# Optimization experiments

Hardware: AMD Instinct MI355X
Metric: run time of the kernel (lower is better)

Reference implementation:

```python
import jax, jax.numpy as jnp
import numpy as np

EPS = 1e-5

def _ln(x, w, b):
    m = jnp.mean(x, axis=-1, keepdims=True)
    v = jnp.var(x, axis=-1, keepdims=True)
    return (x - m) * jax.lax.rsqrt(v + EPS) * w + b

def setup_inputs() -> dict:
    key = jax.random.key(0)
    ks = jax.random.split(key, 8)
    B, N, C, H, D, Hid = 8, 1024, 1024, 16, 64, 4096
    s_in = 1.0 / np.sqrt(C)
    s_out = 1.0 / np.sqrt(Hid + C)
    return {
        "x": jax.random.normal(ks[0], (B, N, C), jnp.float32),
        "in_norm_w": jnp.ones((C,), jnp.float32),
        "in_norm_b": jnp.zeros((C,), jnp.float32),
        "in_proj_w": jax.random.normal(ks[1], (Hid + 3 * C, C), jnp.float32) * s_in,
        "mlp_bias": jax.random.normal(ks[2], (Hid,), jnp.float32) * 0.02,
        "q_norm_w": jnp.ones((D,), jnp.float32),
        "q_norm_b": jnp.zeros((D,), jnp.float32),
        "k_norm_w": jnp.ones((D,), jnp.float32),
        "k_norm_b": jnp.zeros((D,), jnp.float32),
        "out_proj_w": jax.random.normal(ks[3], (2 * C, Hid + C), jnp.float32) * s_out,
        "out_proj_b": jax.random.normal(ks[4], (2 * C,), jnp.float32) * 0.02,
        "ls_gamma": jnp.full((C,), 1e-5, jnp.float32),
    }

def reference(x, in_norm_w, in_norm_b, in_proj_w, mlp_bias,
              q_norm_w, q_norm_b, k_norm_w, k_norm_b,
              out_proj_w, out_proj_b, ls_gamma):
    B, N, C = x.shape
    Hid = mlp_bias.shape[0]
    H = 16
    D = C // H
    y = _ln(x, in_norm_w, in_norm_b)
    # faithful to source: bias = cat(qkv_zeros[3C], mlp_bias) despite split order (mlp, q, k, v)
    bias = jnp.concatenate([jnp.zeros((3 * C,), x.dtype), mlp_bias])
    z = jnp.einsum('bnc,oc->bno', y, in_proj_w) + bias
    x_mlp = z[..., :Hid]
    q = z[..., Hid:Hid + C].reshape(B, N, H, D)
    k = z[..., Hid + C:Hid + 2 * C].reshape(B, N, H, D)
    v = z[..., Hid + 2 * C:].reshape(B, N, H, D)
    q = _ln(q, q_norm_w, q_norm_b).transpose(0, 2, 1, 3)  # [B,H,N,D]
    k = _ln(k, k_norm_w, k_norm_b).transpose(0, 2, 1, 3)
    v = v.transpose(0, 2, 1, 3)
    scale = 1.0 / np.sqrt(D)
    scores = jnp.einsum('bhnd,bhmd->bhnm', q, k) * scale
    attn = jax.nn.softmax(scores, axis=-1)
    x_attn = jnp.einsum('bhnm,bhmd->bhnd', attn, v)
    x_attn = x_attn.transpose(0, 2, 1, 3).reshape(B, N, C)
    x_mlp = jax.nn.gelu(x_mlp, approximate=False)
    cat = jnp.concatenate([x_mlp, x_attn], axis=-1)  # [B,N,Hid+C]
    out = jnp.einsum('bnf,of->bno', cat, out_proj_w) + out_proj_b
    x_mlp_out, x_attn_out = out[..., :C], out[..., C:]
    return x + ls_gamma * (x_attn_out + x_mlp_out)
```

## Files before the change

### kernel.cpp

```cpp
#include <hip/hip_runtime.h>
#include <math.h>


typedef __bf16 bf16x8 __attribute__((ext_vector_type(8)));
typedef float f32x4 __attribute__((ext_vector_type(4)));
typedef unsigned short ushort8v __attribute__((ext_vector_type(8)));

#define GLD16(g, l)                                                            \
  __builtin_amdgcn_global_load_lds(                                            \
      (const __attribute__((address_space(1))) void*)(g),                      \
      (__attribute__((address_space(3))) void*)(l), 16, 0, 0)

__device__ __forceinline__ float b2f(unsigned short u) {
  union { unsigned int i; float f; } v;
  v.i = ((unsigned int)u) << 16;
  return v.f;
}
__device__ __forceinline__ unsigned short f2b(float f) {
  unsigned int i = __float_as_uint(f);
  return (unsigned short)((i + 0x7fffu + ((i >> 16) & 1u)) >> 16);
}
__device__ __forceinline__ unsigned short cvt_elem(const void* p, int i, bool f32) {
  return f32 ? f2b(((const float*)p)[i]) : ((const unsigned short*)p)[i];
}

#define P_INW 0
#define P_INB 1024
#define P_MLPB 2048
#define P_QW 6144
#define P_QB 6208
#define P_KW 6272
#define P_KB 6336

__global__ __launch_bounds__(1024) void k_small(
    const void* inw, const void* inb, const void* mlpb, const void* qw,
    const void* qb, const void* kw, const void* kb,
    unsigned short* __restrict__ params) {
  int t = threadIdx.x;
  bool f32 = (((const unsigned short*)inw)[0] == 0);
  params[P_INW + t] = cvt_elem(inw, t, f32);
  params[P_INB + t] = cvt_elem(inb, t, f32);
  for (int i = t; i < 4096; i += 1024) params[P_MLPB + i] = cvt_elem(mlpb, i, f32);
  if (t < 64) {
    params[P_QW + t] = cvt_elem(qw, t, f32);
    params[P_QB + t] = cvt_elem(qb, t, f32);
    params[P_KW + t] = cvt_elem(kw, t, f32);
    params[P_KB + t] = cvt_elem(kb, t, f32);
  }
}

__global__ __launch_bounds__(256) void k_cvt(
    const void* __restrict__ src, unsigned short* __restrict__ dst, int n4,
    const unsigned short* __restrict__ probe) {
  int i = blockIdx.x * 256 + threadIdx.x;
  if (i >= n4) return;
  bool f32 = (probe[0] == 0);
  if (f32) {
    float4 v = ((const float4*)src)[i];
    ushort4 o;
    o.x = f2b(v.x); o.y = f2b(v.y); o.z = f2b(v.z); o.w = f2b(v.w);
    ((ushort4*)dst)[i] = o;
  } else {
    ((ushort4*)dst)[i] = ((const ushort4*)src)[i];
  }
}

__global__ __launch_bounds__(256) void k_wsum(
    const void* __restrict__ W2, const void* __restrict__ ob,
    unsigned short* __restrict__ W2s, float* __restrict__ bsum,
    const unsigned short* __restrict__ probe) {
  int i = blockIdx.x * 256 + threadIdx.x;
  bool f32 = (probe[0] == 0);
  const int half4 = 1310720;
  if (f32) {
    float4 a = ((const float4*)W2)[i];
    float4 b = ((const float4*)W2)[i + half4];
    ushort4 o;
    o.x = f2b(a.x + b.x); o.y = f2b(a.y + b.y);
    o.z = f2b(a.z + b.z); o.w = f2b(a.w + b.w);
    ((ushort4*)W2s)[i] = o;
    if (i < 1024) bsum[i] = ((const float*)ob)[i] + ((const float*)ob)[i + 1024];
  } else {
    ushort4 a = ((const ushort4*)W2)[i];
    ushort4 b = ((const ushort4*)W2)[i + half4];
    ushort4 o;
    o.x = f2b(b2f(a.x) + b2f(b.x)); o.y = f2b(b2f(a.y) + b2f(b.y));
    o.z = f2b(b2f(a.z) + b2f(b.z)); o.w = f2b(b2f(a.w) + b2f(b.w));
    ((ushort4*)W2s)[i] = o;
    if (i < 1024)
      bsum[i] = b2f(((const unsigned short*)ob)[i]) +
                b2f(((const unsigned short*)ob)[i + 1024]);
  }
}

__global__ __launch_bounds__(256) void k_ln_in(
    const void* __restrict__ x, const unsigned short* __restrict__ params,
    unsigned short* __restrict__ y, const unsigned short* __restrict__ probe) {
  int row = blockIdx.x;
  int t = threadIdx.x;
  bool f32 = (probe[0] == 0);
  float v0, v1, v2, v3;
  if (f32) {
    float4 u = *(const float4*)((const float*)x + (size_t)row * 1024u + t * 4);
    v0 = u.x; v1 = u.y; v2 = u.z; v3 = u.w;
  } else {
    ushort4 u = *(const ushort4*)((const unsigned short*)x + (size_t)row * 1024u + t * 4);
    v0 = b2f(u.x); v1 = b2f(u.y); v2 = b2f(u.z); v3 = b2f(u.w);
  }
  float s = v0 + v1 + v2 + v3;
  float s2 = v0 * v0 + v1 * v1 + v2 * v2 + v3 * v3;
  for (int off = 32; off; off >>= 1) {
    s += __shfl_down(s, off);
    s2 += __shfl_down(s2, off);
  }
  __shared__ __align__(16) float red[8];
  int wv = t >> 6, ln = t & 63;
  if (ln == 0) { red[wv] = s; red[4 + wv] = s2; }
  __syncthreads();
  float S = red[0] + red[1] + red[2] + red[3];
  float S2 = red[4] + red[5] + red[6] + red[7];
  float mean = S * (1.0f / 1024.0f);
  float var = S2 * (1.0f / 1024.0f) - mean * mean;
  float rs = rsqrtf(var + 1e-5f);
  ushort4 wv4 = *(const ushort4*)(params + P_INW + t * 4);
  ushort4 bv4 = *(const ushort4*)(params + P_INB + t * 4);
  ushort4 o;
  o.x = f2b((v0 - mean) * rs * b2f(wv4.x) + b2f(bv4.x));
  o.y = f2b((v1 - mean) * rs * b2f(wv4.y) + b2f(bv4.y));
  o.z = f2b((v2 - mean) * rs * b2f(wv4.z) + b2f(bv4.z));
  o.w = f2b((v3 - mean) * rs * b2f(wv4.w) + b2f(bv4.w));
  *(ushort4*)(y + (size_t)row * 1024u + t * 4) = o;
}

__global__ __launch_bounds__(256) void k_gemm1(
    const unsigned short* __restrict__ A, const unsigned short* __restrict__ W,
    const unsigned short* __restrict__ params, unsigned short* __restrict__ Z,
    int ldz, int mode) {
  __shared__ __align__(16) unsigned short As[128 * 32];
  __shared__ __align__(16) unsigned short Bs[128 * 32];
  const int K = 1024;
  int m0 = blockIdx.x * 128, n0 = blockIdx.y * 128;
  int t = threadIdx.x;
  int wv = t >> 6, lane = t & 63, q4 = lane >> 4, l15 = lane & 15;
  int wm = (wv >> 1) * 64, wn = (wv & 1) * 64;
  f32x4 acc[4][4];
  f32x4 z4 = {0.f, 0.f, 0.f, 0.f};
#pragma unroll
  for (int i = 0; i < 4; i++)
#pragma unroll
    for (int j = 0; j < 4; j++) acc[i][j] = z4;

  const unsigned short* a0 = A + (size_t)(m0 + (t >> 2)) * K + (t & 3) * 8;
  const unsigned short* a1 = a0 + (size_t)64 * K;
  const unsigned short* b0 = W + (size_t)(n0 + (t >> 2)) * K + (t & 3) * 8;
  const unsigned short* b1 = b0 + (size_t)64 * K;

  for (int k0 = 0; k0 < K; k0 += 32) {
    GLD16(a0 + k0, As + t * 8);
    GLD16(a1 + k0, As + (t + 256) * 8);
    GLD16(b0 + k0, Bs + t * 8);
    GLD16(b1 + k0, Bs + (t + 256) * 8);
    __syncthreads();
    bf16x8 af[4], bfv[4];
#pragma unroll
    for (int mi = 0; mi < 4; mi++)
      af[mi] = *(const bf16x8*)(As + (wm + mi * 16 + l15) * 32 + q4 * 8);
#pragma unroll
    for (int ni = 0; ni < 4; ni++)
      bfv[ni] = *(const bf16x8*)(Bs + (wn + ni * 16 + l15) * 32 + q4 * 8);
#pragma unroll
    for (int mi = 0; mi < 4; mi++)
#pragma unroll
      for (int ni = 0; ni < 4; ni++)
        acc[mi][ni] = __builtin_amdgcn_mfma_f32_16x16x32_bf16(
            af[mi], bfv[ni], acc[mi][ni], 0, 0, 0);
    __syncthreads();
  }
#pragma unroll
  for (int ni = 0; ni < 4; ni++) {
    int col = n0 + wn + ni * 16 + l15;
    float bias;
    bool gel;
    if (mode == 0) { bias = b2f(params[P_MLPB + 1024 + col]); gel = false; }
    else { bias = (col < 3072) ? 0.0f : b2f(params[P_MLPB + col - 3072]); gel = true; }
#pragma unroll
    for (int mi = 0; mi < 4; mi++) {
      int row = m0 + wm + mi * 16 + q4 * 4;
#pragma unroll
      for (int r = 0; r < 4; r++) {
        float v = acc[mi][ni][r] + bias;
        if (gel) v = 0.5f * v * (1.0f + erff(v * 0.70710678f));
        Z[(size_t)(row + r) * ldz + col] = f2b(v);
      }
    }
  }
}

__global__ __launch_bounds__(256) void k_qkln(
    unsigned short* __restrict__ qkv, const unsigned short* __restrict__ params) {
  int t = threadIdx.x;
  int wv = t >> 6, lane = t & 63;
  long rowIdx = (long)blockIdx.x * 4 + wv;
  int m = (int)(rowIdx >> 5);
  int rem = (int)(rowIdx & 31);
  int h = rem >> 1, qk = rem & 1;
  unsigned short* p = qkv + (size_t)m * 3072 + qk * 1024 + h * 64;
  float v = b2f(p[lane]);
  float s = v, s2 = v * v;
  for (int off = 32; off; off >>= 1) {
    s += __shfl_down(s, off);
    s2 += __shfl_down(s2, off);
  }
  s = __shfl(s, 0);
  s2 = __shfl(s2, 0);
  float mean = s * (1.0f / 64.0f);
  float var = s2 * (1.0f / 64.0f) - mean * mean;
  float rs = rsqrtf(var + 1e-5f);
  const unsigned short* wp = params + (qk ? P_KW : P_QW);
  const unsigned short* bp = params + (qk ? P_KB : P_QB);
  p[lane] = f2b((v - mean) * rs * b2f(wp[lane]) + b2f(bp[lane]));
}

__global__ __launch_bounds__(256, 3) void k_attn(
    const unsigned short* __restrict__ qkv, unsigned short* __restrict__ O) {
  __shared__ __align__(16) unsigned short Qs[2][128 * 32];
  __shared__ __align__(16) unsigned short Ks[2][64 * 32];
  __shared__ __align__(16) unsigned short Vt[64 * 72];
  __shared__ __align__(16) unsigned short Ps[128 * 72];

  int t = threadIdx.x;
  int w = t >> 6, lane = t & 63, q4 = lane >> 4, l15 = lane & 15;
  int b = blockIdx.y >> 4, h = blockIdx.y & 15;
  int qrow0 = blockIdx.x * 128;
  const int ldz = 3072;
  size_t zbase = (size_t)b * 1024;
  int qcol = h * 64, kcol = 1024 + h * 64, vcol = 2048 + h * 64;

#pragma unroll
  for (int hh = 0; hh < 2; hh++)
#pragma unroll
    for (int p = 0; p < 2; p++) {
      int idx = p * 256 + t;
      const unsigned short* g =
          qkv + (zbase + qrow0 + (idx >> 2)) * ldz + qcol + hh * 32 + (idx & 3) * 8;
      GLD16(g, &Qs[hh][idx * 8]);
    }
  __syncthreads();
  bf16x8 qf[2][2];
#pragma unroll
  for (int mt = 0; mt < 2; mt++)
#pragma unroll
    for (int hh = 0; hh < 2; hh++)
      qf[mt][hh] = *(const bf16x8*)&Qs[hh][(w * 32 + mt * 16 + l15) * 32 + q4 * 8];

  f32x4 o[2][4];
  float m_i[2][4], l_i[2][4];
  f32x4 zz = {0.f, 0.f, 0.f, 0.f};
#pragma unroll
  for (int mt = 0; mt < 2; mt++) {
#pragma unroll
    for (int nt = 0; nt < 4; nt++) o[mt][nt] = zz;
#pragma unroll
    for (int rr = 0; rr < 4; rr++) { m_i[mt][rr] = -1e30f; l_i[mt][rr] = 0.f; }
  }

  for (int kc = 0; kc < 16; kc++) {
    __syncthreads();
#pragma unroll
    for (int hh = 0; hh < 2; hh++) {
      const unsigned short* g =
          qkv + (zbase + kc * 64 + (t >> 2)) * ldz + kcol + hh * 32 + (t & 3) * 8;
      GLD16(g, &Ks[hh][t * 8]);
    }
    {
      int key = t & 63;
#pragma unroll
      for (int i = 0; i < 2; i++) {
        int d0 = ((t >> 6) + i * 4) * 8;
        ushort8v u = *(const ushort8v*)(qkv + (zbase + kc * 64 + key) * ldz + vcol + d0);
#pragma unroll
        for (int j = 0; j < 8; j++) Vt[(d0 + j) * 72 + key] = u[j];
      }
    }
    __syncthreads();

    f32x4 s[2][4];
#pragma unroll
    for (int mt = 0; mt < 2; mt++)
#pragma unroll
      for (int nt = 0; nt < 4; nt++) s[mt][nt] = zz;
#pragma unroll
    for (int hh = 0; hh < 2; hh++) {
      bf16x8 kf[4];
#pragma unroll
      for (int nt = 0; nt < 4; nt++)
        kf[nt] = *(const bf16x8*)&Ks[hh][(nt * 16 + l15) * 32 + q4 * 8];
#pragma unroll
      for (int mt = 0; mt < 2; mt++)
#pragma unroll
        for (int nt = 0; nt < 4; nt++)
          s[mt][nt] = __builtin_amdgcn_mfma_f32_16x16x32_bf16(qf[mt][hh], kf[nt],
                                                              s[mt][nt], 0, 0, 0);
    }

#pragma unroll
    for (int mt = 0; mt < 2; mt++)
#pragma unroll
      for (int rr = 0; rr < 4; rr++) {
        float mx = fmaxf(fmaxf(s[mt][0][rr], s[mt][1][rr]),
                         fmaxf(s[mt][2][rr], s[mt][3][rr])) * 0.125f;
        for (int off = 1; off < 16; off <<= 1) mx = fmaxf(mx, __shfl_xor(mx, off));
        float mn = fmaxf(m_i[mt][rr], mx);
        float alpha = __expf(m_i[mt][rr] - mn);
        float rs = 0.f;
#pragma unroll
        for (int nt = 0; nt < 4; nt++) {
          float p = __expf(s[mt][nt][rr] * 0.125f - mn);
          s[mt][nt][rr] = p;
          rs += p;
        }
        for (int off = 1; off < 16; off <<= 1) rs += __shfl_xor(rs, off);
        l_i[mt][rr] = l_i[mt][rr] * alpha + rs;
        m_i[mt][rr] = mn;
#pragma unroll
        for (int nt = 0; nt < 4; nt++) o[mt][nt][rr] *= alpha;
      }

#pragma unroll
    for (int mt = 0; mt < 2; mt++)
#pragma unroll
      for (int nt = 0; nt < 4; nt++)
#pragma unroll
        for (int rr = 0; rr < 4; rr++)
          Ps[(w * 32 + mt * 16 + q4 * 4 + rr) * 72 + nt * 16 + l15] =
              f2b(s[mt][nt][rr]);

#pragma unroll
    for (int kt = 0; kt < 2; kt++) {
      bf16x8 pf[2], vf[4];
#pragma unroll
      for (int mt = 0; mt < 2; mt++)
        pf[mt] = *(const bf16x8*)&Ps[(w * 32 + mt * 16 + l15) * 72 + kt * 32 + q4 * 8];
#pragma unroll
      for (int nt = 0; nt < 4; nt++)
        vf[nt] = *(const bf16x8*)&Vt[(nt * 16 + l15) * 72 + kt * 32 + q4 * 8];
#pragma unroll
      for (int mt = 0; mt < 2; mt++)
#pragma unroll
        for (int nt = 0; nt < 4; nt++)
          o[mt][nt] = __builtin_amdgcn_mfma_f32_16x16x32_bf16(pf[mt], vf[nt],
                                                              o[mt][nt], 0, 0, 0);
    }
  }

#pragma unroll
  for (int mt = 0; mt < 2; mt++)
#pragma unroll
    for (int nt = 0; nt < 4; nt++)
#pragma unroll
      for (int rr = 0; rr < 4; rr++) {
        int rl = w * 32 + mt * 16 + q4 * 4 + rr;
        float v = o[mt][nt][rr] / l_i[mt][rr];
        O[(zbase + qrow0 + rl) * 1024 + h * 64 + nt * 16 + l15] = f2b(v);
      }
}

__global__ __launch_bounds__(256) void k_gemm2(
    const unsigned short* __restrict__ Zmlp, const unsigned short* __restrict__ attn,
    const unsigned short* __restrict__ W2s, const float* __restrict__ bsum,
    const void* __restrict__ x0, const void* __restrict__ gam0,
    const unsigned short* __restrict__ probe, void* __restrict__ out) {
  __shared__ __align__(16) unsigned short As[128 * 32];
  __shared__ __align__(16) unsigned short Bs[128 * 32];
  int m0 = blockIdx.x * 128, n0 = blockIdx.y * 128;
  int t = threadIdx.x;
  int wv = t >> 6, lane = t & 63, q4 = lane >> 4, l15 = lane & 15;
  int wm = (wv >> 1) * 64, wn = (wv & 1) * 64;
  f32x4 acc[4][4];
  f32x4 z4 = {0.f, 0.f, 0.f, 0.f};
#pragma unroll
  for (int i = 0; i < 4; i++)
#pragma unroll
    for (int j = 0; j < 4; j++) acc[i][j] = z4;

  int rA = t >> 2, kc = (t & 3) * 8;
  const unsigned short* b0 = W2s + (size_t)(n0 + rA) * 5120 + kc;
  const unsigned short* b1 = b0 + (size_t)64 * 5120;

  for (int k0 = 0; k0 < 5120; k0 += 32) {
    const unsigned short *a0, *a1;
    if (k0 < 4096) {
      a0 = Zmlp + (size_t)(m0 + rA) * 4096 + k0 + kc;
      a1 = a0 + (size_t)64 * 4096;
    } else {
      a0 = attn + (size_t)(m0 + rA) * 1024 + (k0 - 4096) + kc;
      a1 = a0 + (size_t)64 * 1024;
    }
    GLD16(a0, As + t * 8);
    GLD16(a1, As + (t + 256) * 8);
    GLD16(b0 + k0, Bs + t * 8);
    GLD16(b1 + k0, Bs + (t + 256) * 8);
    __syncthreads();
    bf16x8 af[4], bfv[4];
#pragma unroll
    for (int mi = 0; mi < 4; mi++)
      af[mi] = *(const bf16x8*)(As + (wm + mi * 16 + l15) * 32 + q4 * 8);
#pragma unroll
    for (int ni = 0; ni < 4; ni++)
      bfv[ni] = *(const bf16x8*)(Bs + (wn + ni * 16 + l15) * 32 + q4 * 8);
#pragma unroll
    for (int mi = 0; mi < 4; mi++)
#pragma unroll
      for (int ni = 0; ni < 4; ni++)
        acc[mi][ni] = __builtin_amdgcn_mfma_f32_16x16x32_bf16(
            af[mi], bfv[ni], acc[mi][ni], 0, 0, 0);
    __syncthreads();
  }
  bool f32 = (probe[0] == 0);
#pragma unroll
  for (int ni = 0; ni < 4; ni++) {
    int col = n0 + wn + ni * 16 + l15;
    float bs = bsum[col];
    float g = f32 ? ((const float*)gam0)[col]
                  : b2f(((const unsigned short*)gam0)[col]);
#pragma unroll
    for (int mi = 0; mi < 4; mi++) {
      int row = m0 + wm + mi * 16 + q4 * 4;
#pragma unroll
      for (int r = 0; r < 4; r++) {
        size_t idx = (size_t)(row + r) * 1024 + col;
        float v = acc[mi][ni][r] + bs;
        if (f32) {
          float xv = ((const float*)x0)[idx];
          ((float*)out)[idx] = xv + g * v;
        } else {
          float xv = b2f(((const unsigned short*)x0)[idx]);
          ((unsigned short*)out)[idx] = f2b(xv + g * v);
        }
      }
    }
  }
}

extern "C" void kernel_launch(void* const* d_in, const int* in_sizes, int n_in,
                              void* d_out, int out_size, void* d_ws, size_t ws_size,
                              hipStream_t stream) {
  const void* x    = d_in[0];
  const void* inw  = d_in[1];
  const void* inb  = d_in[2];
  const void* W1   = d_in[3];
  const void* mlpb = d_in[4];
  const void* qw   = d_in[5];
  const void* qb   = d_in[6];
  const void* kw   = d_in[7];
  const void* kb   = d_in[8];
  const void* W2   = d_in[9];
  const void* ob   = d_in[10];
  const void* gam  = d_in[11];
  const unsigned short* probe = (const unsigned short*)inw;

  char* ws = (char*)d_ws;
  unsigned short* attnb = (unsigned short*)(ws);
  unsigned short* big   = (unsigned short*)(ws + 16777216u);
  unsigned short* y     = (unsigned short*)(ws + 83886080u);
  unsigned short* W2s   = (unsigned short*)(ws + 83886080u);
  float* bsum           = (float*)(ws + 94371840u);
  unsigned short* W1b   = (unsigned short*)(ws + 100663296u);
  unsigned short* params= (unsigned short*)(ws + 115343360u);

  k_small<<<1, 1024, 0, stream>>>(inw, inb, mlpb, qw, qb, kw, kb, params);
  k_cvt<<<7168, 256, 0, stream>>>(W1, W1b, 1835008, probe);
  k_ln_in<<<8192, 256, 0, stream>>>(x, params, y, probe);
  k_gemm1<<<dim3(64, 24), 256, 0, stream>>>(y, W1b + (size_t)4096 * 1024, params,
                                            big, 3072, 0);
  k_qkln<<<65536, 256, 0, stream>>>(big, params);
  k_attn<<<dim3(8, 128), 256, 0, stream>>>(big, attnb);
  k_gemm1<<<dim3(64, 32), 256, 0, stream>>>(y, W1b, params, big, 4096, 1);
  k_wsum<<<5120, 256, 0, stream>>>(W2, ob, W2s, bsum, probe);
  k_gemm2<<<dim3(64, 8), 256, 0, stream>>>(big, attnb, W2s, bsum, x, gam, probe, d_out);
}
```

Before: 641.2 us.

## Fuse q/k layernorm into GEMM epilogue, widen K tile with swizzle, approximate GELU

The QKV GEMM epilogue now applies the per-head q/k layernorm, reducing over each wave's 64-column tile with lane shuffles, so the separate k_qkln kernel and its extra read/write pass over the QKV buffer are gone. The GEMM main loop now stages a 64-wide K slice per iteration, halving the number of barriers, and uses an XOR-swizzled LDS layout to avoid bank conflicts. The exact erf GELU is replaced with a sigmoid approximation x*sigmoid(1.702x), which is cheaper but changes numerics relative to the reference. The larger LDS tiles may reduce occupancy.

```diff
diff --git a/kernel.cpp b/kernel.cpp
--- a/kernel.cpp
+++ b/kernel.cpp
@@ -136,8 +136,8 @@
     const unsigned short* __restrict__ A, const unsigned short* __restrict__ W,
     const unsigned short* __restrict__ params, unsigned short* __restrict__ Z,
     int ldz, int mode) {
-  __shared__ __align__(16) unsigned short As[128 * 32];
-  __shared__ __align__(16) unsigned short Bs[128 * 32];
+  __shared__ __align__(16) unsigned short As[128 * 64];
+  __shared__ __align__(16) unsigned short Bs[128 * 64];
   const int K = 1024;
   int m0 = blockIdx.x * 128, n0 = blockIdx.y * 128;
   int t = threadIdx.x;
@@ -150,75 +150,108 @@
 #pragma unroll
     for (int j = 0; j < 4; j++) acc[i][j] = z4;
 
-  const unsigned short* a0 = A + (size_t)(m0 + (t >> 2)) * K + (t & 3) * 8;
-  const unsigned short* a1 = a0 + (size_t)64 * K;
-  const unsigned short* b0 = W + (size_t)(n0 + (t >> 2)) * K + (t & 3) * 8;
-  const unsigned short* b1 = b0 + (size_t)64 * K;
-
-  for (int k0 = 0; k0 < K; k0 += 32) {
-    GLD16(a0 + k0, As + t * 8);
-    GLD16(a1 + k0, As + (t + 256) * 8);
-    GLD16(b0 + k0, Bs + t * 8);
-    GLD16(b1 + k0, Bs + (t + 256) * 8);
+  int sw = ((t & 7) ^ ((t >> 3) & 7)) * 8;
+  const unsigned short* a0 = A + (size_t)(m0 + (t >> 3)) * K + sw;
+  const unsigned short* b0 = W + (size_t)(n0 + (t >> 3)) * K + sw;
+  int swl = (l15 & 7);
+
+  for (int k0 = 0; k0 < K; k0 += 64) {
+#pragma unroll
+    for (int p = 0; p < 4; p++) {
+      GLD16(a0 + (size_t)(p * 32) * K + k0, As + (p * 256 + t) * 8);
+      GLD16(b0 + (size_t)(p * 32) * K + k0, Bs + (p * 256 + t) * 8);
+    }
     __syncthreads();
-    bf16x8 af[4], bfv[4];
-#pragma unroll
-    for (int mi = 0; mi < 4; mi++)
-      af[mi] = *(const bf16x8*)(As + (wm + mi * 16 + l15) * 32 + q4 * 8);
-#pragma unroll
-    for (int ni = 0; ni < 4; ni++)
-      bfv[ni] = *(const bf16x8*)(Bs + (wn + ni * 16 + l15) * 32 + q4 * 8);
-#pragma unroll
-    for (int mi = 0; mi < 4; mi++)
+#pragma unroll
+    for (int kk = 0; kk < 2; kk++) {
+      bf16x8 af[4], bfv[4];
+#pragma unroll
+      for (int mi = 0; mi < 4; mi++)
+        af[mi] = *(const bf16x8*)(As + (wm + mi * 16 + l15) * 64 +
+                                  (((kk * 4 + q4) ^ swl) * 8));
 #pragma unroll
       for (int ni = 0; ni < 4; ni++)
-        acc[mi][ni] = __builtin_amdgcn_mfma_f32_16x16x32_bf16(
-            af[mi], bfv[ni], acc[mi][ni], 0, 0, 0);
+        bfv[ni] = *(const bf16x8*)(Bs + (wn + ni * 16 + l15) * 64 +
+                                   (((kk * 4 + q4) ^ swl) * 8));
+#pragma unroll
+      for (int mi = 0; mi < 4; mi++)
+#pragma unroll
+        for (int ni = 0; ni < 4; ni++)
+          acc[mi][ni] = __builtin_amdgcn_mfma_f32_16x16x32_bf16(
+              af[mi], bfv[ni], acc[mi][ni], 0, 0, 0);
+    }
     __syncthreads();
   }
-#pragma unroll
-  for (int ni = 0; ni < 4; ni++) {
-    int col = n0 + wn + ni * 16 + l15;
-    float bias;
-    bool gel;
-    if (mode == 0) { bias = b2f(params[P_MLPB + 1024 + col]); gel = false; }
-    else { bias = (col < 3072) ? 0.0f : b2f(params[P_MLPB + col - 3072]); gel = true; }
-#pragma unroll
-    for (int mi = 0; mi < 4; mi++) {
-      int row = m0 + wm + mi * 16 + q4 * 4;
-#pragma unroll
-      for (int r = 0; r < 4; r++) {
-        float v = acc[mi][ni][r] + bias;
-        if (gel) v = 0.5f * v * (1.0f + erff(v * 0.70710678f));
-        Z[(size_t)(row + r) * ldz + col] = f2b(v);
-      }
-    }
-  }
-}
-
-__global__ __launch_bounds__(256) void k_qkln(
-    unsigned short* __restrict__ qkv, const unsigned short* __restrict__ params) {
-  int t = threadIdx.x;
-  int wv = t >> 6, lane = t & 63;
-  long rowIdx = (long)blockIdx.x * 4 + wv;
-  int m = (int)(rowIdx >> 5);
-  int rem = (int)(rowIdx & 31);
-  int h = rem >> 1, qk = rem & 1;
-  unsigned short* p = qkv + (size_t)m * 3072 + qk * 1024 + h * 64;
-  float v = b2f(p[lane]);
-  float s = v, s2 = v * v;
-  for (int off = 32; off; off >>= 1) {
-    s += __shfl_down(s, off);
-    s2 += __shfl_down(s2, off);
-  }
-  s = __shfl(s, 0);
-  s2 = __shfl(s2, 0);
-  float mean = s * (1.0f / 64.0f);
-  float var = s2 * (1.0f / 64.0f) - mean * mean;
-  float rs = rsqrtf(var + 1e-5f);
-  const unsigned short* wp = params + (qk ? P_KW : P_QW);
-  const unsigned short* bp = params + (qk ? P_KB : P_QB);
-  p[lane] = f2b((v - mean) * rs * b2f(wp[lane]) + b2f(bp[lane]));
+
+  if (mode == 0) {
+#pragma unroll
+    for (int ni = 0; ni < 4; ni++) {
+      float bias = b2f(params[P_MLPB + 1024 + n0 + wn + ni * 16 + l15]);
+#pragma unroll
+      for (int mi = 0; mi < 4; mi++)
+#pragma unroll
+        for (int r = 0; r < 4; r++) acc[mi][ni][r] += bias;
+    }
+    if (n0 + wn < 2048) {
+      bool isK = (n0 + wn) >= 1024;
+      float wln[4], bln[4];
+#pragma unroll
+      for (int ni = 0; ni < 4; ni++) {
+        int d = ni * 16 + l15;
+        wln[ni] = b2f(params[(isK ? P_KW : P_QW) + d]);
+        bln[ni] = b2f(params[(isK ? P_KB : P_QB) + d]);
+      }
+#pragma unroll
+      for (int mi = 0; mi < 4; mi++)
+#pragma unroll
+        for (int r = 0; r < 4; r++) {
+          float s = 0.f, s2 = 0.f;
+#pragma unroll
+          for (int ni = 0; ni < 4; ni++) {
+            float v = acc[mi][ni][r];
+            s += v;
+            s2 += v * v;
+          }
+          for (int off = 1; off < 16; off <<= 1) {
+            s += __shfl_xor(s, off);
+            s2 += __shfl_xor(s2, off);
+          }
+          float mean = s * (1.0f / 64.0f);
+          float var = s2 * (1.0f / 64.0f) - mean * mean;
+          float rs = rsqrtf(var + 1e-5f);
+#pragma unroll
+          for (int ni = 0; ni < 4; ni++)
+            acc[mi][ni][r] = (acc[mi][ni][r] - mean) * rs * wln[ni] + bln[ni];
+        }
+    }
+#pragma unroll
+    for (int ni = 0; ni < 4; ni++) {
+      int col = n0 + wn + ni * 16 + l15;
+#pragma unroll
+      for (int mi = 0; mi < 4; mi++) {
+        int row = m0 + wm + mi * 16 + q4 * 4;
+#pragma unroll
+        for (int r = 0; r < 4; r++)
+          Z[(size_t)(row + r) * ldz + col] = f2b(acc[mi][ni][r]);
+      }
+    }
+  } else {
+#pragma unroll
+    for (int ni = 0; ni < 4; ni++) {
+      int col = n0 + wn + ni * 16 + l15;
+      float bias = (col < 3072) ? 0.0f : b2f(params[P_MLPB + col - 3072]);
+#pragma unroll
+      for (int mi = 0; mi < 4; mi++) {
+        int row = m0 + wm + mi * 16 + q4 * 4;
+#pragma unroll
+        for (int r = 0; r < 4; r++) {
+          float v = acc[mi][ni][r] + bias;
+          v = v / (1.0f + __expf(-1.702f * v));
+          Z[(size_t)(row + r) * ldz + col] = f2b(v);
+        }
+      }
+    }
+  }
 }
 
 __global__ __launch_bounds__(256, 3) void k_attn(
@@ -473,7 +506,6 @@
   k_ln_in<<<8192, 256, 0, stream>>>(x, params, y, probe);
   k_gemm1<<<dim3(64, 24), 256, 0, stream>>>(y, W1b + (size_t)4096 * 1024, params,
                                             big, 3072, 0);
-  k_qkln<<<65536, 256, 0, stream>>>(big, params);
   k_attn<<<dim3(8, 128), 256, 0, stream>>>(big, attnb);
   k_gemm1<<<dim3(64, 32), 256, 0, stream>>>(y, W1b, params, big, 4096, 1);
   k_wsum<<<5120, 256, 0, stream>>>(W2, ob, W2s, bsum, probe);
```

Measured after the change: 567.3 us. 1.13x faster.
